# Optimization experiments

Measured on AMD Instinct MI355X. Metric: run time of the kernel, lower is better.

The kernel has to match this reference:

```python
import jax, jax.numpy as jnp
import numpy as np

BN_EPS = 1e-5

def _gin_mlp(h, wa, ba, wb, bb):
    # 2-layer MLP: Linear -> ReLU -> Linear
    return jax.nn.relu(h @ wa + ba) @ wb + bb

def _gin_conv(x, src, dst, n, wa, ba, wb, bb):
    # GIN aggregation: (1+eps)*x + sum_{j->i} x_j, eps=0 (PyG default)
    agg = jax.ops.segment_sum(x[src], dst, num_segments=n)
    return _gin_mlp(x + agg, wa, ba, wb, bb)

def _batchnorm(h, gamma, beta):
    # track_running_stats=False -> always batch stats, biased variance
    mean = jnp.mean(h, axis=0)
    var = jnp.var(h, axis=0)
    return (h - mean) * jax.lax.rsqrt(var + BN_EPS) * gamma + beta

def setup_inputs() -> dict:
    key = jax.random.key(0)
    ks = jax.random.split(key, 8)
    N, E, F, H, C = 100000, 1600000, 64, 64, 10
    s = 0.05
    return {
        "x": jax.random.normal(ks[0], (N, F), dtype=jnp.float32),
        "edge_index": jax.random.randint(ks[1], (2, E), 0, N, dtype=jnp.int64),
        "w1a": jax.random.normal(ks[2], (F, H), dtype=jnp.float32) * s,
        "b1a": jnp.zeros((H,), jnp.float32),
        "w1b": jax.random.normal(ks[3], (H, H), dtype=jnp.float32) * s,
        "b1b": jnp.zeros((H,), jnp.float32),
        "bn_gamma": jnp.ones((H,), jnp.float32),
        "bn_beta": jnp.zeros((H,), jnp.float32),
        "w2a": jax.random.normal(ks[4], (H, H), dtype=jnp.float32) * s,
        "b2a": jnp.zeros((H,), jnp.float32),
        "w2b": jax.random.normal(ks[5], (H, H), dtype=jnp.float32) * s,
        "b2b": jnp.zeros((H,), jnp.float32),
        "lin_w": jax.random.normal(ks[6], (H, C), dtype=jnp.float32) * s,
        "lin_b": jnp.zeros((C,), jnp.float32),
    }

def reference(x, edge_index, w1a, b1a, w1b, b1b, bn_gamma, bn_beta,
              w2a, b2a, w2b, b2b, lin_w, lin_b):
    n = x.shape[0]
    src, dst = edge_index[0], edge_index[1]
    h1 = _gin_conv(x, src, dst, n, w1a, b1a, w1b, b1b)   # [N, H]
    h1 = _batchnorm(h1, bn_gamma, bn_beta)               # relu1 never applied (faithful)
    h2 = _gin_conv(h1, src, dst, n, w2a, b2a, w2b, b2b)  # [N, H]
    return h2 @ lin_w + lin_b                            # [N, C]
```

## Files before the change

kernel.cpp:

```cpp
#include <hip/hip_runtime.h>
#include <hip/hip_fp16.h>

#define H 64
#define CBS 512
#define CB_BITS 9
#define TILE 4096
#define CAP 9216
#define NSTAT 64
#define RPK_BLKS 53

typedef _Float16 f16;
typedef __attribute__((ext_vector_type(8))) _Float16 v8h;
typedef __attribute__((ext_vector_type(4))) float v4f;

__global__ __launch_bounds__(256)
void init_kernel(int* __restrict__ gcursor, float* __restrict__ statsR, int CB) {
    int t = threadIdx.x;
    if (t < CB) gcursor[t * 16] = t * CAP;
    for (int i = t; i < NSTAT * 128; i += 256) statsR[i] = 0.f;
}

__global__ __launch_bounds__(256)
void front_kernel(const int* __restrict__ ei, int* __restrict__ gcursor,
                  int* __restrict__ pairs, int E, int N, int CB, int ntiles,
                  const float* __restrict__ x, f16* __restrict__ xh, int total4,
                  const float* __restrict__ W1a, const float* __restrict__ W1b,
                  const float* __restrict__ W2a, const float* __restrict__ W2b,
                  const float* __restrict__ B2b, const float* __restrict__ LW,
                  const float* __restrict__ LB,
                  f16* __restrict__ pk1a, f16* __restrict__ pk1b,
                  f16* __restrict__ pk2a, f16* __restrict__ pkf,
                  float* __restrict__ bf) {
    __shared__ int sd[256];
    __shared__ int excl[256];
    __shared__ int gbase[256];
    __shared__ int lcur[256];
    __shared__ int stage[TILE];
    __shared__ unsigned char bin8[TILE];
    int b = blockIdx.x;
    int t = threadIdx.x;

    if (b < ntiles) {
        int base = b * TILE;
        int cnt = min(TILE, E - base);
        sd[t] = 0;
        __syncthreads();
        for (int i = t; i < cnt; i += 256) {
            int s = ei[base + i];
            int d = ei[E + base + i];
            if ((unsigned)s < (unsigned)N && (unsigned)d < (unsigned)N)
                atomicAdd(&sd[d >> CB_BITS], 1);
        }
        __syncthreads();
        int v = sd[t];
        __syncthreads();
        for (int off = 1; off < 256; off <<= 1) {
            int add = (t >= off) ? sd[t - off] : 0;
            __syncthreads();
            sd[t] += add;
            __syncthreads();
        }
        int ex = sd[t] - v;
        excl[t] = ex;
        lcur[t] = ex;
        if (t < CB && v > 0) gbase[t] = atomicAdd(&gcursor[t * 16], v);
        int tot = sd[255];
        __syncthreads();
        for (int i = t; i < cnt; i += 256) {
            int s = ei[base + i];
            int d = ei[E + base + i];
            if ((unsigned)s < (unsigned)N && (unsigned)d < (unsigned)N) {
                int cb = d >> CB_BITS;
                int pos = atomicAdd(&lcur[cb], 1);
                stage[pos] = s | ((d & (CBS - 1)) << 17);
                bin8[pos] = (unsigned char)cb;
            }
        }
        __syncthreads();
        for (int i = t; i < tot; i += 256) {
            int b8 = bin8[i];
            pairs[gbase[b8] + (i - excl[b8])] = stage[i];
        }
        return;
    }
    b -= ntiles;
    if (b < RPK_BLKS) {
        int tt = b * 256 + t;
        if (tt < 12288) {
            int m = tt >> 12;
            int e = tt & 4095;
            int j = e & 7, lane = (e >> 3) & 63, ks = (e >> 9) & 1, nt = e >> 10;
            int row = ks * 32 + ((lane >> 4) & 3) * 8 + j;
            int col = nt * 16 + (lane & 15);
            const float* W = (m == 0) ? W1a : (m == 1) ? W1b : W2a;
            f16* P = (m == 0) ? pk1a : (m == 1) ? pk1b : pk2a;
            P[e] = (f16)W[row * 64 + col];
        } else if (tt < 13312) {
            int e = tt - 12288;
            int j = e & 7, lane = (e >> 3) & 63, ks = e >> 9;
            int row = ks * 32 + ((lane >> 4) & 3) * 8 + j;
            int col = lane & 15;
            float a = 0.f;
            if (col < 10)
                for (int m = 0; m < H; ++m) a = fmaf(W2b[row * 64 + m], LW[m * 10 + col], a);
            pkf[e] = (f16)a;
        } else if (tt < 13322) {
            int c = tt - 13312;
            float a = LB[c];
            for (int m = 0; m < H; ++m) a = fmaf(B2b[m], LW[m * 10 + c], a);
            bf[c] = a;
        }
        return;
    }
    b -= RPK_BLKS;
    int i = b * 256 + t;
    if (i >= total4) return;
    float4 v = ((const float4*)x)[i];
    f16 h0 = (f16)v.x, h1 = (f16)v.y, h2 = (f16)v.z, h3 = (f16)v.w;
    ushort4 pk;
    pk.x = *(unsigned short*)&h0; pk.y = *(unsigned short*)&h1;
    pk.z = *(unsigned short*)&h2; pk.w = *(unsigned short*)&h3;
    ((ushort4*)xh)[i] = pk;
}

__global__ __launch_bounds__(256)
void bucket_csr_kernel(const int* __restrict__ pairs, const int* __restrict__ gcursor,
                       int* __restrict__ ebuf, int* __restrict__ rowptr, int N, int CB) {
    __shared__ int hist[CBS];
    __shared__ int cur[CBS];
    __shared__ int sd[256];
    __shared__ int carry_s;
    int b = blockIdx.x;
    int t = threadIdx.x;
    int c_t = (t < CB) ? (gcursor[t * 16] - t * CAP) : 0;
    sd[t] = c_t; __syncthreads();
    for (int off = 1; off < 256; off <<= 1) {
        int add = (t >= off) ? sd[t - off] : 0;
        __syncthreads();
        sd[t] += add;
        __syncthreads();
    }
    int cnt = gcursor[b * 16] - b * CAP;
    int gb = sd[b] - cnt;
    if (b == 0 && t == 0) rowptr[N] = sd[255];
    __syncthreads();

    int pb = b * CAP;
    for (int i = t; i < CBS; i += 256) hist[i] = 0;
    if (t == 0) carry_s = 0;
    __syncthreads();
    for (int i = t; i < cnt; i += 256)
        atomicAdd(&hist[(pairs[pb + i] >> 17) & (CBS - 1)], 1);
    __syncthreads();
    for (int start = 0; start < CBS; start += 256) {
        int v = hist[start + t];
        sd[t] = v; __syncthreads();
        for (int off = 1; off < 256; off <<= 1) {
            int add = (t >= off) ? sd[t - off] : 0;
            __syncthreads();
            sd[t] += add;
            __syncthreads();
        }
        int ex = sd[t] - v + carry_s;
        cur[start + t] = ex;
        int node = b * CBS + start + t;
        if (node < N) rowptr[node] = gb + ex;
        __syncthreads();
        if (t == 0) carry_s += sd[255];
        __syncthreads();
    }
    for (int i = t; i < cnt; i += 256) {
        int p = pairs[pb + i];
        int pos = atomicAdd(&cur[(p >> 17) & (CBS - 1)], 1);
        ebuf[gb + pos] = p & 0x1FFFF;
    }
}

__global__ __launch_bounds__(256)
void gather1_kernel(const f16* __restrict__ xh, const int* __restrict__ rowptr,
                    const int* __restrict__ ebuf, f16* __restrict__ bufA,
                    int N, int Em1) {
    int wid = (int)(((long long)blockIdx.x * blockDim.x + threadIdx.x) >> 6);
    int lane = threadIdx.x & 63;
    int g = lane >> 3, fl = lane & 7;
    int node = wid * 8 + g;
    bool vn = node < N;
    int p0 = 0, deg = 0;
    if (vn) {
        p0 = rowptr[node];
        deg = rowptr[node + 1] - p0;
    }
    float a[8];
    {
        v8h s = {};
        if (vn) s = *(const v8h*)(xh + ((size_t)node << 6) + fl * 8);
#pragma unroll
        for (int j = 0; j < 8; ++j) a[j] = (float)s[j];
    }
    int k = 0;
    if (deg >= 16) {
        int idxA[8];
#pragma unroll
        for (int q = 0; q < 8; ++q) idxA[q] = ebuf[p0 + q];
        for (; k + 16 <= deg; k += 8) {
            int idxB[8];
#pragma unroll
            for (int q = 0; q < 8; ++q) idxB[q] = ebuf[p0 + k + 8 + q];
#pragma unroll
            for (int q = 0; q < 8; ++q) {
                v8h v = *(const v8h*)(xh + ((size_t)idxA[q] << 6) + fl * 8);
#pragma unroll
                for (int j = 0; j < 8; ++j) a[j] += (float)v[j];
            }
#pragma unroll
            for (int q = 0; q < 8; ++q) idxA[q] = idxB[q];
        }
#pragma unroll
        for (int q = 0; q < 8; ++q) {
            v8h v = *(const v8h*)(xh + ((size_t)idxA[q] << 6) + fl * 8);
#pragma unroll
            for (int j = 0; j < 8; ++j) a[j] += (float)v[j];
        }
        k += 8;
    } else if (deg >= 8) {
        int idxA[8];
#pragma unroll
        for (int q = 0; q < 8; ++q) idxA[q] = ebuf[p0 + q];
#pragma unroll
        for (int q = 0; q < 8; ++q) {
            v8h v = *(const v8h*)(xh + ((size_t)idxA[q] << 6) + fl * 8);
#pragma unroll
            for (int j = 0; j < 8; ++j) a[j] += (float)v[j];
        }
        k = 8;
    }
    if (k < deg) {
        int idx[8];
#pragma unroll
        for (int q = 0; q < 8; ++q) idx[q] = ebuf[min(p0 + k + q, Em1)];
#pragma unroll
        for (int q = 0; q < 8; ++q) {
            if (k + q < deg) {
                v8h v = *(const v8h*)(xh + ((size_t)idx[q] << 6) + fl * 8);
#pragma unroll
                for (int j = 0; j < 8; ++j) a[j] += (float)v[j];
            }
        }
    }
    if (vn) {
        v8h o;
#pragma unroll
        for (int j = 0; j < 8; ++j) o[j] = (f16)a[j];
        *(v8h*)(bufA + ((size_t)node << 6) + fl * 8) = o;
    }
}

__global__ __launch_bounds__(256)
void gather2_kernel(const f16* __restrict__ h1p, const float* __restrict__ statsR,
                    const float* __restrict__ gamma, const float* __restrict__ beta,
                    const int* __restrict__ rowptr, const int* __restrict__ ebuf,
                    f16* __restrict__ bufC, int N, int Em1, float n) {
    __shared__ float s_scale[64];
    __shared__ float s_shift[64];
    int t = threadIdx.x;
    if (t < 64) {
        float s = 0.f, s2 = 0.f;
#pragma unroll 8
        for (int r = 0; r < NSTAT; ++r) {
            s  += statsR[r * 128 + t];
            s2 += statsR[r * 128 + 64 + t];
        }
        float mean = s / n;
        float var = fmaxf(s2 / n - mean * mean, 0.f);
        float sc = gamma[t] * rsqrtf(var + 1e-5f);
        s_scale[t] = sc;
        s_shift[t] = beta[t] - mean * sc;
    }
    __syncthreads();

    int wid = (int)(((long long)blockIdx.x * blockDim.x + t) >> 6);
    int lane = t & 63;
    int g = lane >> 3, fl = lane & 7;
    int node = wid * 8 + g;
    bool vn = node < N;
    int p0 = 0, deg = 0;
    if (vn) {
        p0 = rowptr[node];
        deg = rowptr[node + 1] - p0;
    }
    float a[8];
    {
        v8h s = {};
        if (vn) s = *(const v8h*)(h1p + ((size_t)node << 6) + fl * 8);
#pragma unroll
        for (int j = 0; j < 8; ++j) a[j] = (float)s[j];
    }
    int k = 0;
    if (deg >= 16) {
        int idxA[8];
#pragma unroll
        for (int q = 0; q < 8; ++q) idxA[q] = ebuf[p0 + q];
        for (; k + 16 <= deg; k += 8) {
            int idxB[8];
#pragma unroll
            for (int q = 0; q < 8; ++q) idxB[q] = ebuf[p0 + k + 8 + q];
#pragma unroll
            for (int q = 0; q < 8; ++q) {
                v8h v = *(const v8h*)(h1p + ((size_t)idxA[q] << 6) + fl * 8);
#pragma unroll
                for (int j = 0; j < 8; ++j) a[j] += (float)v[j];
            }
#pragma unroll
            for (int q = 0; q < 8; ++q) idxA[q] = idxB[q];
        }
#pragma unroll
        for (int q = 0; q < 8; ++q) {
            v8h v = *(const v8h*)(h1p + ((size_t)idxA[q] << 6) + fl * 8);
#pragma unroll
            for (int j = 0; j < 8; ++j) a[j] += (float)v[j];
        }
        k += 8;
    } else if (deg >= 8) {
        int idxA[8];
#pragma unroll
        for (int q = 0; q < 8; ++q) idxA[q] = ebuf[p0 + q];
#pragma unroll
        for (int q = 0; q < 8; ++q) {
            v8h v = *(const v8h*)(h1p + ((size_t)idxA[q] << 6) + fl * 8);
#pragma unroll
            for (int j = 0; j < 8; ++j) a[j] += (float)v[j];
        }
        k = 8;
    }
    if (k < deg) {
        int idx[8];
#pragma unroll
        for (int q = 0; q < 8; ++q) idx[q] = ebuf[min(p0 + k + q, Em1)];
#pragma unroll
        for (int q = 0; q < 8; ++q) {
            if (k + q < deg) {
                v8h v = *(const v8h*)(h1p + ((size_t)idx[q] << 6) + fl * 8);
#pragma unroll
                for (int j = 0; j < 8; ++j) a[j] += (float)v[j];
            }
        }
    }
    if (vn) {
        float degp1 = (float)(deg + 1);
        v8h o;
#pragma unroll
        for (int j = 0; j < 8; ++j)
            o[j] = (f16)(a[j] * s_scale[fl * 8 + j] + degp1 * s_shift[fl * 8 + j]);
        *(v8h*)(bufC + ((size_t)node << 6) + fl * 8) = o;
    }
}

__global__ __launch_bounds__(256)
void mlp1_kernel(const f16* __restrict__ bufA, f16* __restrict__ h1p,
                 const f16* __restrict__ pk1a, const f16* __restrict__ pk1b,
                 const float* __restrict__ B1a, const float* __restrict__ B1b,
                 float* __restrict__ statsR, int N) {
    __shared__ f16 Su[4][16 * 72];
    __shared__ f16 Sh[4][16 * 72];
    __shared__ float red[2][4][64];
    int t = threadIdx.x, wv = t >> 6, lane = t & 63;
    int quad = lane >> 4, r16 = lane & 15;
    int node0 = blockIdx.x * 64 + wv * 16;
    int nodeA = node0 + r16;

    v8h a0 = {}, a1 = {};
    if (nodeA < N) {
        a0 = *(const v8h*)(bufA + (size_t)nodeA * 64 + quad * 8);
        a1 = *(const v8h*)(bufA + (size_t)nodeA * 64 + 32 + quad * 8);
    }
#pragma unroll
    for (int nt = 0; nt < 4; ++nt) {
        v8h b0 = *(const v8h*)(pk1a + (((nt * 2 + 0) * 64 + lane) << 3));
        v8h b1 = *(const v8h*)(pk1a + (((nt * 2 + 1) * 64 + lane) << 3));
        v4f c = {0.f, 0.f, 0.f, 0.f};
        c = __builtin_amdgcn_mfma_f32_16x16x32_f16(a0, b0, c, 0, 0, 0);
        c = __builtin_amdgcn_mfma_f32_16x16x32_f16(a1, b1, c, 0, 0, 0);
        float bias = B1a[nt * 16 + r16];
#pragma unroll
        for (int reg = 0; reg < 4; ++reg)
            Su[wv][(quad * 4 + reg) * 72 + nt * 16 + r16] = (f16)fmaxf(c[reg] + bias, 0.f);
    }
    __syncthreads();
    v8h u0 = *(const v8h*)(&Su[wv][r16 * 72 + quad * 8]);
    v8h u1 = *(const v8h*)(&Su[wv][r16 * 72 + 32 + quad * 8]);
#pragma unroll
    for (int nt = 0; nt < 4; ++nt) {
        v8h b0 = *(const v8h*)(pk1b + (((nt * 2 + 0) * 64 + lane) << 3));
        v8h b1 = *(const v8h*)(pk1b + (((nt * 2 + 1) * 64 + lane) << 3));
        v4f c = {0.f, 0.f, 0.f, 0.f};
        c = __builtin_amdgcn_mfma_f32_16x16x32_f16(u0, b0, c, 0, 0, 0);
        c = __builtin_amdgcn_mfma_f32_16x16x32_f16(u1, b1, c, 0, 0, 0);
        float bias = B1b[nt * 16 + r16];
#pragma unroll
        for (int reg = 0; reg < 4; ++reg) {
            int row = quad * 4 + reg;
            bool valid = (node0 + row) < N;
            Sh[wv][row * 72 + nt * 16 + r16] = valid ? (f16)(c[reg] + bias) : (f16)0;
        }
    }
    __syncthreads();
    for (int i = lane; i < 1024; i += 64) {
        int row = i >> 6, col = i & 63;
        int node = node0 + row;
        if (node < N) h1p[(size_t)node * 64 + col] = Sh[wv][row * 72 + col];
    }
    float s = 0.f, s2 = 0.f;
#pragma unroll
    for (int row = 0; row < 16; ++row) {
        float v = (float)Sh[wv][row * 72 + lane];
        s += v;
        s2 = fmaf(v, v, s2);
    }
    red[0][wv][lane] = s;
    red[1][wv][lane] = s2;
    __syncthreads();
    if (wv == 0) {
        float ts  = (red[0][0][lane] + red[0][1][lane]) + (red[0][2][lane] + red[0][3][lane]);
        float ts2 = (red[1][0][lane] + red[1][1][lane]) + (red[1][2][lane] + red[1][3][lane]);
        float* st = statsR + (size_t)(blockIdx.x & (NSTAT - 1)) * 128;
        unsafeAtomicAdd(&st[lane], ts);
        unsafeAtomicAdd(&st[64 + lane], ts2);
    }
}

__global__ __launch_bounds__(256)
void mlp2_kernel(const f16* __restrict__ bufC,
                 const f16* __restrict__ pk2a, const f16* __restrict__ pkf,
                 const float* __restrict__ B2a, const float* __restrict__ bf,
                 float* __restrict__ out, int N) {
    __shared__ f16 Su[4][16 * 72];
    int t = threadIdx.x, wv = t >> 6, lane = t & 63;
    int quad = lane >> 4, r16 = lane & 15;
    int node0 = blockIdx.x * 64 + wv * 16;
    int nodeA = node0 + r16;

    v8h a0 = {}, a1 = {};
    if (nodeA < N) {
        a0 = *(const v8h*)(bufC + (size_t)nodeA * 64 + quad * 8);
        a1 = *(const v8h*)(bufC + (size_t)nodeA * 64 + 32 + quad * 8);
    }
#pragma unroll
    for (int nt = 0; nt < 4; ++nt) {
        v8h b0 = *(const v8h*)(pk2a + (((nt * 2 + 0) * 64 + lane) << 3));
        v8h b1 = *(const v8h*)(pk2a + (((nt * 2 + 1) * 64 + lane) << 3));
        v4f c = {0.f, 0.f, 0.f, 0.f};
        c = __builtin_amdgcn_mfma_f32_16x16x32_f16(a0, b0, c, 0, 0, 0);
        c = __builtin_amdgcn_mfma_f32_16x16x32_f16(a1, b1, c, 0, 0, 0);
        float bias = B2a[nt * 16 + r16];
#pragma unroll
        for (int reg = 0; reg < 4; ++reg)
            Su[wv][(quad * 4 + reg) * 72 + nt * 16 + r16] = (f16)fmaxf(c[reg] + bias, 0.f);
    }
    __syncthreads();
    v8h u0 = *(const v8h*)(&Su[wv][r16 * 72 + quad * 8]);
    v8h u1 = *(const v8h*)(&Su[wv][r16 * 72 + 32 + quad * 8]);
    v8h b0 = *(const v8h*)(pkf + ((0 * 64 + lane) << 3));
    v8h b1 = *(const v8h*)(pkf + ((1 * 64 + lane) << 3));
    v4f c = {0.f, 0.f, 0.f, 0.f};
    c = __builtin_amdgcn_mfma_f32_16x16x32_f16(u0, b0, c, 0, 0, 0);
    c = __builtin_amdgcn_mfma_f32_16x16x32_f16(u1, b1, c, 0, 0, 0);
    if (r16 < 10) {
        float bias = bf[r16];
#pragma unroll
        for (int reg = 0; reg < 4; ++reg) {
            int node = node0 + quad * 4 + reg;
            if (node < N) out[(size_t)node * 10 + r16] = c[reg] + bias;
        }
    }
}

extern "C" void kernel_launch(void* const* d_in, const int* in_sizes, int n_in,
                              void* d_out, int out_size, void* d_ws, size_t ws_size,
                              hipStream_t stream) {
    const float* x    = (const float*)d_in[0];
    const int*   ei   = (const int*)d_in[1];
    const float* w1a  = (const float*)d_in[2];
    const float* b1a  = (const float*)d_in[3];
    const float* w1b  = (const float*)d_in[4];
    const float* b1b  = (const float*)d_in[5];
    const float* bng  = (const float*)d_in[6];
    const float* bnb  = (const float*)d_in[7];
    const float* w2a  = (const float*)d_in[8];
    const float* b2a  = (const float*)d_in[9];
    const float* w2b  = (const float*)d_in[10];
    const float* b2b  = (const float*)d_in[11];
    const float* linw = (const float*)d_in[12];
    const float* linb = (const float*)d_in[13];

    int N = in_sizes[0] / H;
    int E = in_sizes[1] / 2;
    int CB = (N + CBS - 1) / CBS;

    size_t NH = (size_t)N * H;
    char*  wsb    = (char*)d_ws;
    f16*   xh     = (f16*)wsb;
    f16*   bufA   = (f16*)(wsb + NH * 2);
    f16*   bufC   = (f16*)(wsb + NH * 4);
    float* stats  = (float*)(wsb + NH * 6);
    float* scale  = stats + 128;
    float* shiftv = stats + 192;
    float* bf     = stats + 256;
    f16*   pk1a   = (f16*)(bf + 16);
    f16*   pk1b   = pk1a + 4096;
    f16*   pk2a   = pk1b + 4096;
    f16*   pkf    = pk2a + 4096;
    int*   gcursor= (int*)(pkf + 1024);
    int*   rowptr = gcursor + 256 * 16;
    int*   ebuf   = rowptr + (N + 1);
    int*   pairs  = ebuf + E;
    float* statsR = (float*)(pairs + (size_t)CB * CAP);

    int ntiles = (E + TILE - 1) / TILE;
    int total4 = (int)(NH / 4);
    int cvtblocks = (total4 + 255) / 256;
    int mblocks = (N + 63) / 64;
    int nwaves = (N + 7) / 8;
    int gblocks = (int)(((long long)nwaves * 64 + 255) / 256);

    init_kernel<<<1, 256, 0, stream>>>(gcursor, statsR, CB);
    front_kernel<<<ntiles + RPK_BLKS + cvtblocks, 256, 0, stream>>>(
        ei, gcursor, pairs, E, N, CB, ntiles,
        x, xh, total4,
        w1a, w1b, w2a, w2b, b2b, linw, linb,
        pk1a, pk1b, pk2a, pkf, bf);
    bucket_csr_kernel<<<CB, 256, 0, stream>>>(pairs, gcursor, ebuf, rowptr, N, CB);

    gather1_kernel<<<gblocks, 256, 0, stream>>>(xh, rowptr, ebuf, bufA, N, E - 1);
    mlp1_kernel<<<mblocks, 256, 0, stream>>>(bufA, bufA, pk1a, pk1b, b1a, b1b, statsR, N);

    gather2_kernel<<<gblocks, 256, 0, stream>>>(
        bufA, statsR, bng, bnb, rowptr, ebuf, bufC, N, E - 1, (float)N);
    mlp2_kernel<<<mblocks, 256, 0, stream>>>(bufC, pk2a, pkf, b2a, bf, (float*)d_out, N);
}
```

Measured before the change: 230.7 us.

## Fuse neighbor gather into MLP kernels via per-wave LDS staging

```diff
diff --git a/kernel.cpp b/kernel.cpp
--- a/kernel.cpp
+++ b/kernel.cpp
@@ -177,202 +177,94 @@
 }
 
 __global__ __launch_bounds__(256)
-void gather1_kernel(const f16* __restrict__ xh, const int* __restrict__ rowptr,
-                    const int* __restrict__ ebuf, f16* __restrict__ bufA,
-                    int N, int Em1) {
-    int wid = (int)(((long long)blockIdx.x * blockDim.x + threadIdx.x) >> 6);
-    int lane = threadIdx.x & 63;
+void g1mlp1_kernel(const f16* __restrict__ xh, const int* __restrict__ rowptr,
+                   const int* __restrict__ ebuf, f16* __restrict__ h1p,
+                   const f16* __restrict__ pk1a, const f16* __restrict__ pk1b,
+                   const float* __restrict__ B1a, const float* __restrict__ B1b,
+                   float* __restrict__ statsR, int N, int Em1) {
+    __shared__ f16 aggS[4][16 * 72];
+    __shared__ float red[2][4][64];
+    int t = threadIdx.x, wv = t >> 6, lane = t & 63;
     int g = lane >> 3, fl = lane & 7;
-    int node = wid * 8 + g;
-    bool vn = node < N;
-    int p0 = 0, deg = 0;
-    if (vn) {
-        p0 = rowptr[node];
-        deg = rowptr[node + 1] - p0;
-    }
-    float a[8];
-    {
-        v8h s = {};
-        if (vn) s = *(const v8h*)(xh + ((size_t)node << 6) + fl * 8);
-#pragma unroll
-        for (int j = 0; j < 8; ++j) a[j] = (float)s[j];
-    }
-    int k = 0;
-    if (deg >= 16) {
-        int idxA[8];
-#pragma unroll
-        for (int q = 0; q < 8; ++q) idxA[q] = ebuf[p0 + q];
-        for (; k + 16 <= deg; k += 8) {
-            int idxB[8];
-#pragma unroll
-            for (int q = 0; q < 8; ++q) idxB[q] = ebuf[p0 + k + 8 + q];
+    int quad = lane >> 4, r16 = lane & 15;
+    int node0 = blockIdx.x * 64;
+    int nbase = node0 + wv * 16;
+    f16* agg = &aggS[wv][0];
+
+    for (int r = 0; r < 2; ++r) {
+        int nl = r * 8 + g;
+        int node = nbase + nl;
+        bool vn = node < N;
+        int p0 = 0, deg = 0;
+        if (vn) {
+            p0 = rowptr[node];
+            deg = rowptr[node + 1] - p0;
+        }
+        float a[8];
+        {
+            v8h s = {};
+            if (vn) s = *(const v8h*)(xh + ((size_t)node << 6) + fl * 8);
+#pragma unroll
+            for (int j = 0; j < 8; ++j) a[j] = (float)s[j];
+        }
+        int k = 0;
+        if (deg >= 16) {
+            int idxA[8];
+#pragma unroll
+            for (int q = 0; q < 8; ++q) idxA[q] = ebuf[p0 + q];
+            for (; k + 16 <= deg; k += 8) {
+                int idxB[8];
+#pragma unroll
+                for (int q = 0; q < 8; ++q) idxB[q] = ebuf[p0 + k + 8 + q];
+#pragma unroll
+                for (int q = 0; q < 8; ++q) {
+                    v8h v = *(const v8h*)(xh + ((size_t)idxA[q] << 6) + fl * 8);
+#pragma unroll
+                    for (int j = 0; j < 8; ++j) a[j] += (float)v[j];
+                }
+#pragma unroll
+                for (int q = 0; q < 8; ++q) idxA[q] = idxB[q];
+            }
 #pragma unroll
             for (int q = 0; q < 8; ++q) {
                 v8h v = *(const v8h*)(xh + ((size_t)idxA[q] << 6) + fl * 8);
 #pragma unroll
                 for (int j = 0; j < 8; ++j) a[j] += (float)v[j];
             }
-#pragma unroll
-            for (int q = 0; q < 8; ++q) idxA[q] = idxB[q];
-        }
-#pragma unroll
-        for (int q = 0; q < 8; ++q) {
-            v8h v = *(const v8h*)(xh + ((size_t)idxA[q] << 6) + fl * 8);
-#pragma unroll
-            for (int j = 0; j < 8; ++j) a[j] += (float)v[j];
-        }
-        k += 8;
-    } else if (deg >= 8) {
-        int idxA[8];
-#pragma unroll
-        for (int q = 0; q < 8; ++q) idxA[q] = ebuf[p0 + q];
-#pragma unroll
-        for (int q = 0; q < 8; ++q) {
-            v8h v = *(const v8h*)(xh + ((size_t)idxA[q] << 6) + fl * 8);
-#pragma unroll
-            for (int j = 0; j < 8; ++j) a[j] += (float)v[j];
-        }
-        k = 8;
-    }
-    if (k < deg) {
-        int idx[8];
-#pragma unroll
-        for (int q = 0; q < 8; ++q) idx[q] = ebuf[min(p0 + k + q, Em1)];
-#pragma unroll
-        for (int q = 0; q < 8; ++q) {
-            if (k + q < deg) {
-                v8h v = *(const v8h*)(xh + ((size_t)idx[q] << 6) + fl * 8);
+            k += 8;
+        } else if (deg >= 8) {
+            int idxA[8];
+#pragma unroll
+            for (int q = 0; q < 8; ++q) idxA[q] = ebuf[p0 + q];
+#pragma unroll
+            for (int q = 0; q < 8; ++q) {
+                v8h v = *(const v8h*)(xh + ((size_t)idxA[q] << 6) + fl * 8);
 #pragma unroll
                 for (int j = 0; j < 8; ++j) a[j] += (float)v[j];
             }
-        }
-    }
-    if (vn) {
+            k = 8;
+        }
+        if (k < deg) {
+            int idx[8];
+#pragma unroll
+            for (int q = 0; q < 8; ++q) idx[q] = ebuf[min(p0 + k + q, Em1)];
+#pragma unroll
+            for (int q = 0; q < 8; ++q) {
+                if (k + q < deg) {
+                    v8h v = *(const v8h*)(xh + ((size_t)idx[q] << 6) + fl * 8);
+#pragma unroll
+                    for (int j = 0; j < 8; ++j) a[j] += (float)v[j];
+                }
+            }
+        }
         v8h o;
 #pragma unroll
         for (int j = 0; j < 8; ++j) o[j] = (f16)a[j];
-        *(v8h*)(bufA + ((size_t)node << 6) + fl * 8) = o;
-    }
-}
-
-__global__ __launch_bounds__(256)
-void gather2_kernel(const f16* __restrict__ h1p, const float* __restrict__ statsR,
-                    const float* __restrict__ gamma, const float* __restrict__ beta,
-                    const int* __restrict__ rowptr, const int* __restrict__ ebuf,
-                    f16* __restrict__ bufC, int N, int Em1, float n) {
-    __shared__ float s_scale[64];
-    __shared__ float s_shift[64];
-    int t = threadIdx.x;
-    if (t < 64) {
-        float s = 0.f, s2 = 0.f;
-#pragma unroll 8
-        for (int r = 0; r < NSTAT; ++r) {
-            s  += statsR[r * 128 + t];
-            s2 += statsR[r * 128 + 64 + t];
-        }
-        float mean = s / n;
-        float var = fmaxf(s2 / n - mean * mean, 0.f);
-        float sc = gamma[t] * rsqrtf(var + 1e-5f);
-        s_scale[t] = sc;
-        s_shift[t] = beta[t] - mean * sc;
-    }
-    __syncthreads();
-
-    int wid = (int)(((long long)blockIdx.x * blockDim.x + t) >> 6);
-    int lane = t & 63;
-    int g = lane >> 3, fl = lane & 7;
-    int node = wid * 8 + g;
-    bool vn = node < N;
-    int p0 = 0, deg = 0;
-    if (vn) {
-        p0 = rowptr[node];
-        deg = rowptr[node + 1] - p0;
-    }
-    float a[8];
-    {
-        v8h s = {};
-        if (vn) s = *(const v8h*)(h1p + ((size_t)node << 6) + fl * 8);
-#pragma unroll
-        for (int j = 0; j < 8; ++j) a[j] = (float)s[j];
-    }
-    int k = 0;
-    if (deg >= 16) {
-        int idxA[8];
-#pragma unroll
-        for (int q = 0; q < 8; ++q) idxA[q] = ebuf[p0 + q];
-        for (; k + 16 <= deg; k += 8) {
-            int idxB[8];
-#pragma unroll
-            for (int q = 0; q < 8; ++q) idxB[q] = ebuf[p0 + k + 8 + q];
-#pragma unroll
-            for (int q = 0; q < 8; ++q) {
-                v8h v = *(const v8h*)(h1p + ((size_t)idxA[q] << 6) + fl * 8);
-#pragma unroll
-                for (int j = 0; j < 8; ++j) a[j] += (float)v[j];
-            }
-#pragma unroll
-            for (int q = 0; q < 8; ++q) idxA[q] = idxB[q];
-        }
-#pragma unroll
-        for (int q = 0; q < 8; ++q) {
-            v8h v = *(const v8h*)(h1p + ((size_t)idxA[q] << 6) + fl * 8);
-#pragma unroll
-            for (int j = 0; j < 8; ++j) a[j] += (float)v[j];
-        }
-        k += 8;
-    } else if (deg >= 8) {
-        int idxA[8];
-#pragma unroll
-        for (int q = 0; q < 8; ++q) idxA[q] = ebuf[p0 + q];
-#pragma unroll
-        for (int q = 0; q < 8; ++q) {
-            v8h v = *(const v8h*)(h1p + ((size_t)idxA[q] << 6) + fl * 8);
-#pragma unroll
-            for (int j = 0; j < 8; ++j) a[j] += (float)v[j];
-        }
-        k = 8;
-    }
-    if (k < deg) {
-        int idx[8];
-#pragma unroll
-        for (int q = 0; q < 8; ++q) idx[q] = ebuf[min(p0 + k + q, Em1)];
-#pragma unroll
-        for (int q = 0; q < 8; ++q) {
-            if (k + q < deg) {
-                v8h v = *(const v8h*)(h1p + ((size_t)idx[q] << 6) + fl * 8);
-#pragma unroll
-                for (int j = 0; j < 8; ++j) a[j] += (float)v[j];
-            }
-        }
-    }
-    if (vn) {
-        float degp1 = (float)(deg + 1);
-        v8h o;
-#pragma unroll
-        for (int j = 0; j < 8; ++j)
-            o[j] = (f16)(a[j] * s_scale[fl * 8 + j] + degp1 * s_shift[fl * 8 + j]);
-        *(v8h*)(bufC + ((size_t)node << 6) + fl * 8) = o;
-    }
-}
-
-__global__ __launch_bounds__(256)
-void mlp1_kernel(const f16* __restrict__ bufA, f16* __restrict__ h1p,
-                 const f16* __restrict__ pk1a, const f16* __restrict__ pk1b,
-                 const float* __restrict__ B1a, const float* __restrict__ B1b,
-                 float* __restrict__ statsR, int N) {
-    __shared__ f16 Su[4][16 * 72];
-    __shared__ f16 Sh[4][16 * 72];
-    __shared__ float red[2][4][64];
-    int t = threadIdx.x, wv = t >> 6, lane = t & 63;
-    int quad = lane >> 4, r16 = lane & 15;
-    int node0 = blockIdx.x * 64 + wv * 16;
-    int nodeA = node0 + r16;
-
-    v8h a0 = {}, a1 = {};
-    if (nodeA < N) {
-        a0 = *(const v8h*)(bufA + (size_t)nodeA * 64 + quad * 8);
-        a1 = *(const v8h*)(bufA + (size_t)nodeA * 64 + 32 + quad * 8);
-    }
+        *(v8h*)(agg + nl * 72 + fl * 8) = o;
+    }
+
+    v8h a0 = *(const v8h*)(agg + r16 * 72 + quad * 8);
+    v8h a1 = *(const v8h*)(agg + r16 * 72 + 32 + quad * 8);
 #pragma unroll
     for (int nt = 0; nt < 4; ++nt) {
         v8h b0 = *(const v8h*)(pk1a + (((nt * 2 + 0) * 64 + lane) << 3));
@@ -383,11 +275,10 @@
         float bias = B1a[nt * 16 + r16];
 #pragma unroll
         for (int reg = 0; reg < 4; ++reg)
-            Su[wv][(quad * 4 + reg) * 72 + nt * 16 + r16] = (f16)fmaxf(c[reg] + bias, 0.f);
-    }
-    __syncthreads();
-    v8h u0 = *(const v8h*)(&Su[wv][r16 * 72 + quad * 8]);
-    v8h u1 = *(const v8h*)(&Su[wv][r16 * 72 + 32 + quad * 8]);
+            agg[(quad * 4 + reg) * 72 + nt * 16 + r16] = (f16)fmaxf(c[reg] + bias, 0.f);
+    }
+    v8h u0 = *(const v8h*)(agg + r16 * 72 + quad * 8);
+    v8h u1 = *(const v8h*)(agg + r16 * 72 + 32 + quad * 8);
 #pragma unroll
     for (int nt = 0; nt < 4; ++nt) {
         v8h b0 = *(const v8h*)(pk1b + (((nt * 2 + 0) * 64 + lane) << 3));
@@ -399,20 +290,19 @@
 #pragma unroll
         for (int reg = 0; reg < 4; ++reg) {
             int row = quad * 4 + reg;
-            bool valid = (node0 + row) < N;
-            Sh[wv][row * 72 + nt * 16 + r16] = valid ? (f16)(c[reg] + bias) : (f16)0;
-        }
-    }
-    __syncthreads();
+            bool valid = (nbase + row) < N;
+            agg[row * 72 + nt * 16 + r16] = valid ? (f16)(c[reg] + bias) : (f16)0;
+        }
+    }
     for (int i = lane; i < 1024; i += 64) {
         int row = i >> 6, col = i & 63;
-        int node = node0 + row;
-        if (node < N) h1p[(size_t)node * 64 + col] = Sh[wv][row * 72 + col];
+        int node = nbase + row;
+        if (node < N) h1p[(size_t)node * 64 + col] = agg[row * 72 + col];
     }
     float s = 0.f, s2 = 0.f;
 #pragma unroll
     for (int row = 0; row < 16; ++row) {
-        float v = (float)Sh[wv][row * 72 + lane];
+        float v = (float)agg[row * 72 + lane];
         s += v;
         s2 = fmaf(v, v, s2);
     }
@@ -429,21 +319,116 @@
 }
 
 __global__ __launch_bounds__(256)
-void mlp2_kernel(const f16* __restrict__ bufC,
-                 const f16* __restrict__ pk2a, const f16* __restrict__ pkf,
-                 const float* __restrict__ B2a, const float* __restrict__ bf,
-                 float* __restrict__ out, int N) {
-    __shared__ f16 Su[4][16 * 72];
+void g2mlp2_kernel(const f16* __restrict__ h1p, const float* __restrict__ statsR,
+                   const float* __restrict__ gamma, const float* __restrict__ beta,
+                   const int* __restrict__ rowptr, const int* __restrict__ ebuf,
+                   const f16* __restrict__ pk2a, const f16* __restrict__ pkf,
+                   const float* __restrict__ B2a, const float* __restrict__ bf,
+                   float* __restrict__ out, int N, int Em1, float n) {
+    __shared__ f16 aggS[4][16 * 72];
+    __shared__ float s_scale[64];
+    __shared__ float s_shift[64];
     int t = threadIdx.x, wv = t >> 6, lane = t & 63;
+    int g = lane >> 3, fl = lane & 7;
     int quad = lane >> 4, r16 = lane & 15;
-    int node0 = blockIdx.x * 64 + wv * 16;
-    int nodeA = node0 + r16;
-
-    v8h a0 = {}, a1 = {};
-    if (nodeA < N) {
-        a0 = *(const v8h*)(bufC + (size_t)nodeA * 64 + quad * 8);
-        a1 = *(const v8h*)(bufC + (size_t)nodeA * 64 + 32 + quad * 8);
-    }
+    int node0 = blockIdx.x * 64;
+    int nbase = node0 + wv * 16;
+    f16* agg = &aggS[wv][0];
+
+    if (t < 64) {
+        float s = 0.f, s2 = 0.f;
+#pragma unroll 8
+        for (int r = 0; r < NSTAT; ++r) {
+            s  += statsR[r * 128 + t];
+            s2 += statsR[r * 128 + 64 + t];
+        }
+        float mean = s / n;
+        float var = fmaxf(s2 / n - mean * mean, 0.f);
+        float sc = gamma[t] * rsqrtf(var + 1e-5f);
+        s_scale[t] = sc;
+        s_shift[t] = beta[t] - mean * sc;
+    }
+    __syncthreads();
+
+    float sc[8], sh[8];
+#pragma unroll
+    for (int j = 0; j < 8; ++j) { sc[j] = s_scale[fl * 8 + j]; sh[j] = s_shift[fl * 8 + j]; }
+
+    for (int r = 0; r < 2; ++r) {
+        int nl = r * 8 + g;
+        int node = nbase + nl;
+        bool vn = node < N;
+        int p0 = 0, deg = 0;
+        if (vn) {
+            p0 = rowptr[node];
+            deg = rowptr[node + 1] - p0;
+        }
+        float a[8];
+        {
+            v8h s = {};
+            if (vn) s = *(const v8h*)(h1p + ((size_t)node << 6) + fl * 8);
+#pragma unroll
+            for (int j = 0; j < 8; ++j) a[j] = (float)s[j];
+        }
+        int k = 0;
+        if (deg >= 16) {
+            int idxA[8];
+#pragma unroll
+            for (int q = 0; q < 8; ++q) idxA[q] = ebuf[p0 + q];
+            for (; k + 16 <= deg; k += 8) {
+                int idxB[8];
+#pragma unroll
+                for (int q = 0; q < 8; ++q) idxB[q] = ebuf[p0 + k + 8 + q];
+#pragma unroll
+                for (int q = 0; q < 8; ++q) {
+                    v8h v = *(const v8h*)(h1p + ((size_t)idxA[q] << 6) + fl * 8);
+#pragma unroll
+                    for (int j = 0; j < 8; ++j) a[j] += (float)v[j];
+                }
+#pragma unroll
+                for (int q = 0; q < 8; ++q) idxA[q] = idxB[q];
+            }
+#pragma unroll
+            for (int q = 0; q < 8; ++q) {
+                v8h v = *(const v8h*)(h1p + ((size_t)idxA[q] << 6) + fl * 8);
+#pragma unroll
+                for (int j = 0; j < 8; ++j) a[j] += (float)v[j];
+            }
+            k += 8;
+        } else if (deg >= 8) {
+            int idxA[8];
+#pragma unroll
+            for (int q = 0; q < 8; ++q) idxA[q] = ebuf[p0 + q];
+#pragma unroll
+            for (int q = 0; q < 8; ++q) {
+                v8h v = *(const v8h*)(h1p + ((size_t)idxA[q] << 6) + fl * 8);
+#pragma unroll
+                for (int j = 0; j < 8; ++j) a[j] += (float)v[j];
+            }
+            k = 8;
+        }
+        if (k < deg) {
+            int idx[8];
+#pragma unroll
+            for (int q = 0; q < 8; ++q) idx[q] = ebuf[min(p0 + k + q, Em1)];
+#pragma unroll
+            for (int q = 0; q < 8; ++q) {
+                if (k + q < deg) {
+                    v8h v = *(const v8h*)(h1p + ((size_t)idx[q] << 6) + fl * 8);
+#pragma unroll
+                    for (int j = 0; j < 8; ++j) a[j] += (float)v[j];
+                }
+            }
+        }
+        float degp1 = (float)(deg + 1);
+        v8h o;
+#pragma unroll
+        for (int j = 0; j < 8; ++j) o[j] = (f16)(a[j] * sc[j] + degp1 * sh[j]);
+        *(v8h*)(agg + nl * 72 + fl * 8) = o;
+    }
+
+    v8h a0 = *(const v8h*)(agg + r16 * 72 + quad * 8);
+    v8h a1 = *(const v8h*)(agg + r16 * 72 + 32 + quad * 8);
 #pragma unroll
     for (int nt = 0; nt < 4; ++nt) {
         v8h b0 = *(const v8h*)(pk2a + (((nt * 2 + 0) * 64 + lane) << 3));
@@ -454,11 +439,10 @@
         float bias = B2a[nt * 16 + r16];
 #pragma unroll
         for (int reg = 0; reg < 4; ++reg)
-            Su[wv][(quad * 4 + reg) * 72 + nt * 16 + r16] = (f16)fmaxf(c[reg] + bias, 0.f);
-    }
-    __syncthreads();
-    v8h u0 = *(const v8h*)(&Su[wv][r16 * 72 + quad * 8]);
-    v8h u1 = *(const v8h*)(&Su[wv][r16 * 72 + 32 + quad * 8]);
+            agg[(quad * 4 + reg) * 72 + nt * 16 + r16] = (f16)fmaxf(c[reg] + bias, 0.f);
+    }
+    v8h u0 = *(const v8h*)(agg + r16 * 72 + quad * 8);
+    v8h u1 = *(const v8h*)(agg + r16 * 72 + 32 + quad * 8);
     v8h b0 = *(const v8h*)(pkf + ((0 * 64 + lane) << 3));
     v8h b1 = *(const v8h*)(pkf + ((1 * 64 + lane) << 3));
     v4f c = {0.f, 0.f, 0.f, 0.f};
@@ -468,7 +452,7 @@
         float bias = bf[r16];
 #pragma unroll
         for (int reg = 0; reg < 4; ++reg) {
-            int node = node0 + quad * 4 + reg;
+            int node = nbase + quad * 4 + reg;
             if (node < N) out[(size_t)node * 10 + r16] = c[reg] + bias;
         }
     }
@@ -499,11 +483,8 @@
     size_t NH = (size_t)N * H;
     char*  wsb    = (char*)d_ws;
     f16*   xh     = (f16*)wsb;
-    f16*   bufA   = (f16*)(wsb + NH * 2);
-    f16*   bufC   = (f16*)(wsb + NH * 4);
+    f16*   h1p    = (f16*)(wsb + NH * 2);
     float* stats  = (float*)(wsb + NH * 6);
-    float* scale  = stats + 128;
-    float* shiftv = stats + 192;
     float* bf     = stats + 256;
     f16*   pk1a   = (f16*)(bf + 16);
     f16*   pk1b   = pk1a + 4096;
@@ -519,8 +500,6 @@
     int total4 = (int)(NH / 4);
     int cvtblocks = (total4 + 255) / 256;
     int mblocks = (N + 63) / 64;
-    int nwaves = (N + 7) / 8;
-    int gblocks = (int)(((long long)nwaves * 64 + 255) / 256);
 
     init_kernel<<<1, 256, 0, stream>>>(gcursor, statsR, CB);
     front_kernel<<<ntiles + RPK_BLKS + cvtblocks, 256, 0, stream>>>(
@@ -530,10 +509,9 @@
         pk1a, pk1b, pk2a, pkf, bf);
     bucket_csr_kernel<<<CB, 256, 0, stream>>>(pairs, gcursor, ebuf, rowptr, N, CB);
 
-    gather1_kernel<<<gblocks, 256, 0, stream>>>(xh, rowptr, ebuf, bufA, N, E - 1);
-    mlp1_kernel<<<mblocks, 256, 0, stream>>>(bufA, bufA, pk1a, pk1b, b1a, b1b, statsR, N);
-
-    gather2_kernel<<<gblocks, 256, 0, stream>>>(
-        bufA, statsR, bng, bnb, rowptr, ebuf, bufC, N, E - 1, (float)N);
-    mlp2_kernel<<<mblocks, 256, 0, stream>>>(bufC, pk2a, pkf, b2a, bf, (float*)d_out, N);
+    g1mlp1_kernel<<<mblocks, 256, 0, stream>>>(
+        xh, rowptr, ebuf, h1p, pk1a, pk1b, b1a, b1b, statsR, N, E - 1);
+    g2mlp2_kernel<<<mblocks, 256, 0, stream>>>(
+        h1p, statsR, bng, bnb, rowptr, ebuf, pk2a, pkf, b2a, bf,
+        (float*)d_out, N, E - 1, (float)N);
 }
```

Result: slower. 239.6 us (+3.8%).
